# Kernel tuning notes

Hardware: AMD Instinct MI355X
Metric: run time of the kernel (lower is better)

The kernel has to match this reference:

```python
import jax, jax.numpy as jnp
import numpy as np

VOCAB, D, S, T, B, E, C = 21128, 768, 50, 5, 512, 128, 10


def gcn(x, edges, W, b):
    # GCNConv with self-loops and symmetric normalization. x: [S, D]
    N = x.shape[0]
    loop = jnp.arange(N)
    src = jnp.concatenate([edges[0], loop])
    dst = jnp.concatenate([edges[1], loop])
    deg = jax.ops.segment_sum(jnp.ones_like(src, dtype=x.dtype), dst, num_segments=N)
    dinv = jax.lax.rsqrt(jnp.maximum(deg, 1e-12))
    norm = dinv[src] * dinv[dst]
    h = x @ W  # [S, 10]
    out = jax.ops.segment_sum(h[src] * norm[:, None], dst, num_segments=N)
    return out + b


def mpm(self_f, cross_f, assign, W1, b1, W2, b2):
    # multi-perspective matching, broadcast over leading dims; node dim = -2
    a = assign * self_f
    c = assign * cross_f
    num = jnp.sum(a * c, axis=-1)
    den = jnp.maximum(jnp.linalg.norm(a, axis=-1) * jnp.linalg.norm(c, axis=-1), 1e-8)
    cos = num / den
    bshape = jnp.broadcast_shapes(self_f.shape[:-2], cross_f.shape[:-2])
    sf = jnp.broadcast_to(self_f, bshape + self_f.shape[-2:])
    h = jnp.concatenate([cos[..., None], sf], axis=-1)  # [..., S, 11]
    h = jax.nn.relu(h @ W1 + b1) @ W2 + b2  # [..., S, 20]
    return jnp.max(h, axis=-2)  # [..., 20]


def setup_inputs() -> dict:
    key = jax.random.key(0)
    ks = jax.random.split(key, 20)
    inp = {
        "context_input": jax.random.randint(ks[0], (B, T, S), 0, VOCAB),
        "response_input": jax.random.randint(ks[1], (B, S), 0, VOCAB),
        "context_graph_adjs": jax.random.randint(ks[2], (B, T, 2, E), 0, S),
        "response_graph_adj": jax.random.randint(ks[3], (B, 2, E), 0, S),
        "word_emb": jax.random.normal(ks[4], (VOCAB, D), jnp.float32) * 0.02,
        "conv_W": jax.random.normal(ks[5], (D, C), jnp.float32) * 0.05,
        "conv_b": jnp.zeros((C,), jnp.float32),
        "cross_w": jax.random.uniform(ks[6], (D, C), jnp.float32),
        "attention_coef": jax.random.uniform(ks[7], (S, S), jnp.float32),
        "assign_weight": jax.random.uniform(ks[8], (S, C), jnp.float32),
        "mp_W1": jax.random.normal(ks[9], (C + 1, 20), jnp.float32) * 0.3,
        "mp_b1": jnp.zeros((20,), jnp.float32),
        "mp_W2": jax.random.normal(ks[10], (20, 20), jnp.float32) * 0.2,
        "mp_b2": jnp.zeros((20,), jnp.float32),
        "ffn_W1": jax.random.normal(ks[11], (80, 40), jnp.float32) * 0.1,
        "ffn_b1": jnp.zeros((40,), jnp.float32),
        "ffn_W2": jax.random.normal(ks[12], (40, 1), jnp.float32) * 0.2,
        "ffn_b2": jnp.zeros((1,), jnp.float32),
    }
    return inp


def reference(context_input, response_input, context_graph_adjs, response_graph_adj,
              word_emb, conv_W, conv_b, cross_w, attention_coef, assign_weight,
              mp_W1, mp_b1, mp_W2, mp_b2, ffn_W1, ffn_b1, ffn_W2, ffn_b2):
    ctx = word_emb[context_input]      # [B, T, S, D]
    resp = word_emb[response_input]    # [B, S, D]

    gcn_b = jax.vmap(gcn, in_axes=(0, 0, None, None))
    resp_gcn = gcn_b(resp, response_graph_adj, conv_W, conv_b)                      # [B, S, C]
    ctx_gcn = jax.vmap(gcn_b, in_axes=(0, 0, None, None))(ctx, context_graph_adjs, conv_W, conv_b)  # [B, T, S, C]

    # cross features: utterance cross comes from response, response cross from utterance
    u_cross = jnp.einsum('ps,bsk->bpk', attention_coef, resp @ cross_w)   # [B, S, C]
    r_cross = jnp.einsum('ps,btsk->btpk', attention_coef, ctx @ cross_w)  # [B, T, S, C]

    g_u = mpm(ctx_gcn, u_cross[:, None], assign_weight, mp_W1, mp_b1, mp_W2, mp_b2)       # [B, T, 20]
    g_r = mpm(resp_gcn[:, None], r_cross, assign_weight, mp_W1, mp_b1, mp_W2, mp_b2)      # [B, T, 20]

    feat = jnp.concatenate([g_u, g_r, g_u * g_r, jnp.abs(g_u - g_r)], axis=-1)  # [B, T, 80]
    logits = jax.nn.relu(feat @ ffn_W1 + ffn_b1) @ ffn_W2 + ffn_b2              # [B, T, 1]
    return jax.nn.sigmoid(jnp.sum(logits, axis=1))                              # [B, 1]
```

## Files before the change

### kernel.cpp

```cpp
#include <hip/hip_runtime.h>
#include <math.h>

#define VOCAB 21128
#define DD 768
#define SS 50
#define TT 5
#define BB 512
#define EE 128
#define CC 10
#define V20 (VOCAB * 20)
#define NG 2560

__global__ __launch_bounds__(512) void k_vocab(const float* __restrict__ emb,
                                               const float* __restrict__ Wconv,
                                               const float* __restrict__ Wcross,
                                               float* __restrict__ hvp) {
    __shared__ float tile[8][64][21];
    const int wv = threadIdx.x >> 6, lane = threadIdx.x & 63;
    const int rowbase = blockIdx.x * 64;
    const int rsub = lane >> 2, m = lane & 3;

    float acc[20];
#pragma unroll
    for (int c = 0; c < 20; c++) acc[c] = 0.f;

    const int d0w = blockIdx.y * 384 + __builtin_amdgcn_readfirstlane(wv * 48);

    for (int chunk = 0; chunk < 3; ++chunk) {
        const int d0 = d0w + chunk * 16;
#pragma unroll
        for (int it = 0; it < 4; ++it) {
            int row = it * 16 + rsub;
            long r = rowbase + row;
            if (r >= VOCAB) r = VOCAB - 1;
            const float4 v = *(const float4*)(emb + r * DD + d0 + m * 4);
            tile[wv][row][m * 4 + 0] = v.x;
            tile[wv][row][m * 4 + 1] = v.y;
            tile[wv][row][m * 4 + 2] = v.z;
            tile[wv][row][m * 4 + 3] = v.w;
        }
#pragma unroll
        for (int d = 0; d < 16; ++d) {
            float e = tile[wv][lane][d];
            const float* wc = Wconv + (d0 + d) * 10;
            const float* wx = Wcross + (d0 + d) * 10;
#pragma unroll
            for (int c = 0; c < 10; c++) {
                acc[c] = fmaf(e, wc[c], acc[c]);
                acc[10 + c] = fmaf(e, wx[c], acc[10 + c]);
            }
        }
    }

    __syncthreads();
    float* pp = &tile[0][0][0];
#pragma unroll
    for (int c = 0; c < 20; c++) pp[wv * 1280 + lane * 20 + c] = acc[c];
    __syncthreads();
    float* outp = hvp + (long)blockIdx.y * V20;
    for (int i = threadIdx.x; i < 1280; i += 512) {
        int row = i / 20;
        long r = rowbase + row;
        if (r < VOCAB) {
            float s = 0.f;
#pragma unroll
            for (int w = 0; w < 8; ++w) s += pp[w * 1280 + i];
            outp[r * 20 + (i - row * 20)] = s;
        }
    }
}

__device__ __forceinline__ void wave_gcn(const int* __restrict__ tb,
                                         const int* __restrict__ ab,
                                         const float* __restrict__ hvp,
                                         const float* __restrict__ convb,
                                         const float (*attT)[51],
                                         float (*hsL)[21], float (*agg)[21], int* dgW,
                                         int lane, float* gcn, float* ax) {
    const int e1s = ab[lane], e2s = ab[lane + 64];
    const int e1d = ab[EE + lane], e2d = ab[EE + lane + 64];
    const int myTok = (lane < SS) ? tb[lane] : 0;

    dgW[lane] = 0;
    atomicAdd(&dgW[e1d], 1);
    atomicAdd(&dgW[e2d], 1);

    const float4* hv4 = (const float4*)hvp;
#pragma unroll
    for (int it = 0; it < 4; ++it) {
        const int idx = it * 64 + lane;
        int row = idx / 5;
        const int q = idx - row * 5;
        const int rowc = (row < SS) ? row : (SS - 1);
        const int t = __shfl(myTok, rowc);
        if (idx < SS * 5) {
            const float4 a = hv4[(long)t * 5 + q];
            const float4 bq = hv4[(long)(VOCAB * 5) + (long)t * 5 + q];
            float* dst = &hsL[row][q * 4];
            dst[0] = a.x + bq.x; dst[1] = a.y + bq.y;
            dst[2] = a.z + bq.z; dst[3] = a.w + bq.w;
        }
    }

    float dv = 0.f;
    if (lane < SS) dv = rsqrtf((float)(dgW[lane] + 1));

#pragma unroll
    for (int it = 0; it < 8; ++it) {
        const int i = it * 64 + lane;
        const int r = i / 10, c = i - r * 10;
        if (i < SS * 10) agg[r][c] = 0.f;
    }
    const float n1 = __shfl(dv, e1s) * __shfl(dv, e1d);
    const float n2 = __shfl(dv, e2s) * __shfl(dv, e2d);
#pragma unroll
    for (int c = 0; c < CC; c++) atomicAdd(&agg[e1d][c], hsL[e1s][c] * n1);
#pragma unroll
    for (int c = 0; c < CC; c++) atomicAdd(&agg[e2d][c], hsL[e2s][c] * n2);

    const int p = lane;
#pragma unroll
    for (int c = 0; c < CC; c++) { gcn[c] = 0.f; ax[c] = 0.f; }
    if (p < SS) {
        const float dp2 = dv * dv;
#pragma unroll
        for (int c = 0; c < CC; c++) gcn[c] = agg[p][c] + hsL[p][c] * dp2 + convb[c];
#pragma unroll 5
        for (int s = 0; s < SS; ++s) {
            const float a = attT[s][p];
#pragma unroll
            for (int c = 0; c < CC; c++) ax[c] = fmaf(a, hsL[s][10 + c], ax[c]);
        }
    }
}

__global__ __launch_bounds__(128) void k_resp(const int* __restrict__ rtok,
                                              const int* __restrict__ radj,
                                              const float* __restrict__ hvp,
                                              const float* __restrict__ convb,
                                              const float* __restrict__ att,
                                              float* __restrict__ srxu) {
    __shared__ float attT[SS][51];
    __shared__ float hsL[2][SS][21];
    __shared__ float aggL[2][SS][21];
    __shared__ int dgS[2][64];
    const int tid = threadIdx.x, wv = tid >> 6, lane = tid & 63;
    const int b = blockIdx.x * 2 + wv;

    for (int i = tid; i < SS * SS; i += 128) { int p = i / SS, s = i - p * SS; attT[s][p] = att[i]; }
    __syncthreads();

    float gcn[CC], ax[CC];
    wave_gcn(rtok + (long)b * SS, radj + (long)b * 2 * EE, hvp, convb, attT,
             hsL[wv], aggL[wv], dgS[wv], lane, gcn, ax);

    if (lane < SS) {
        float* o = srxu + (long)b * 1000 + lane * 20;
#pragma unroll
        for (int c = 0; c < CC; c++) { o[c] = gcn[c]; o[10 + c] = ax[c]; }
    }
}

__global__ __launch_bounds__(128) void k_utt(const int* __restrict__ ctok,
                                             const int* __restrict__ cadj,
                                             const float* __restrict__ hvp,
                                             const float* __restrict__ convb,
                                             const float* __restrict__ att,
                                             const float* __restrict__ assign,
                                             const float* __restrict__ W1, const float* __restrict__ b1,
                                             const float* __restrict__ W2, const float* __restrict__ b2,
                                             const float* __restrict__ srxu,
                                             float* __restrict__ guG,
                                             float* __restrict__ grG) {
    __shared__ float attT[SS][51];
    __shared__ float W2T[20][21];
    __shared__ float asgL[SS][11];
    __shared__ float hsL[2][SS][21];
    __shared__ float h1L[2][SS][21];
    __shared__ int dgS[2][64];
    const int tid = threadIdx.x, wv = tid >> 6, lane = tid & 63;
    const int g = blockIdx.x * 2 + wv;
    const int b = g / TT;

    for (int i = tid; i < SS * SS; i += 128) { int p = i / SS, s = i - p * SS; attT[s][p] = att[i]; }
    for (int i = tid; i < 400; i += 128) W2T[i % 20][i / 20] = W2[i];
    for (int i = tid; i < SS * CC; i += 128) asgL[i / CC][i % CC] = assign[i];
    __syncthreads();

    float gcn[CC], ax[CC];
    wave_gcn(ctok + (long)g * SS, cadj + (long)g * 2 * EE, hvp, convb, attT,
             hsL[wv], h1L[wv], dgS[wv], lane, gcn, ax);

    const int p = lane;
    float srv[CC], xuv[CC];
#pragma unroll
    for (int c = 0; c < CC; c++) { srv[c] = 0.f; xuv[c] = 0.f; }
    if (p < SS) {
        const float4* sp4 = (const float4*)(srxu + (long)b * 1000 + p * 20);
        const float4 t0 = sp4[0], t1 = sp4[1], t2 = sp4[2], t3 = sp4[3], t4 = sp4[4];
        srv[0] = t0.x; srv[1] = t0.y; srv[2] = t0.z; srv[3] = t0.w;
        srv[4] = t1.x; srv[5] = t1.y; srv[6] = t1.z; srv[7] = t1.w;
        srv[8] = t2.x; srv[9] = t2.y;
        xuv[0] = t2.z; xuv[1] = t2.w;
        xuv[2] = t3.x; xuv[3] = t3.y; xuv[4] = t3.z; xuv[5] = t3.w;
        xuv[6] = t4.x; xuv[7] = t4.y; xuv[8] = t4.z; xuv[9] = t4.w;
    }

    const int j = lane % 20;
    const int grp = lane / 20;
    float w2r[20];
#pragma unroll
    for (int k = 0; k < 20; k++) w2r[k] = W2T[j][k];

#pragma unroll
    for (int which = 0; which < 2; ++which) {
        if (p < SS) {
            float self[CC], cro[CC];
#pragma unroll
            for (int c = 0; c < CC; c++) {
                self[c] = which ? srv[c] : gcn[c];
                cro[c] = which ? ax[c] : xuv[c];
            }
            float num = 0.f, na = 0.f, nc2 = 0.f;
#pragma unroll
            for (int c = 0; c < CC; c++) {
                float av = asgL[p][c];
                float a = av * self[c];
                float cx = av * cro[c];
                num = fmaf(a, cx, num);
                na = fmaf(a, a, na);
                nc2 = fmaf(cx, cx, nc2);
            }
            float cosv = num / fmaxf(sqrtf(na) * sqrtf(nc2), 1e-8f);
            float h1[20];
#pragma unroll
            for (int q = 0; q < 20; q++) h1[q] = fmaf(cosv, W1[q], b1[q]);
#pragma unroll
            for (int k = 0; k < CC; k++) {
                float sv = self[k];
#pragma unroll
                for (int q = 0; q < 20; q++) h1[q] = fmaf(sv, W1[(k + 1) * 20 + q], h1[q]);
            }
#pragma unroll
            for (int q = 0; q < 20; q++) h1L[wv][p][q] = fmaxf(h1[q], 0.f);
        }

        float part = -1e30f;
        if (grp < 3) {
            const int s0 = grp * 17;
            const int s1 = (grp == 2) ? SS : (s0 + 17);
            for (int s = s0; s < s1; ++s) {
                float t = 0.f;
#pragma unroll
                for (int k = 0; k < 20; k++) t = fmaf(h1L[wv][s][k], w2r[k], t);
                part = fmaxf(part, t);
            }
        }
        const float a0 = __shfl(part, j);
        const float a1 = __shfl(part, j + 20);
        const float a2 = __shfl(part, j + 40);
        if (lane < 20) {
            float h2 = fmaxf(fmaxf(a0, a1), a2) + b2[lane];
            (which ? grG : guG)[(long)g * 20 + lane] = h2;
        }
    }
}

__global__ __launch_bounds__(64) void k_final(const float* __restrict__ g_u, const float* __restrict__ g_r,
                                              const float* __restrict__ W1, const float* __restrict__ b1,
                                              const float* __restrict__ W2, const float* __restrict__ b2,
                                              float* __restrict__ out) {
    const int b = blockIdx.x, lane = threadIdx.x;
    float ssum = 0.f;
    for (int t = 0; t < TT; t++) {
        const float* gu = g_u + ((long)b * TT + t) * 20;
        const float* gr = g_r + ((long)b * TT + t) * 20;
        float feat[80];
#pragma unroll
        for (int k = 0; k < 20; k++) {
            float u = gu[k], r = gr[k];
            feat[k] = u;
            feat[20 + k] = r;
            feat[40 + k] = u * r;
            feat[60 + k] = fabsf(u - r);
        }
        if (lane < 40) {
            float hv = b1[lane];
#pragma unroll
            for (int k = 0; k < 80; k++) hv = fmaf(feat[k], W1[k * 40 + lane], hv);
            ssum += fmaxf(hv, 0.f) * W2[lane];
        }
    }
    for (int off = 32; off; off >>= 1) ssum += __shfl_xor(ssum, off);
    if (lane == 0) out[b] = 1.f / (1.f + expf(-(ssum + (float)TT * b2[0])));
}

extern "C" void kernel_launch(void* const* d_in, const int* in_sizes, int n_in,
                              void* d_out, int out_size, void* d_ws, size_t ws_size,
                              hipStream_t stream) {
    (void)in_sizes; (void)n_in; (void)out_size; (void)ws_size;
    const int* ctx_tok = (const int*)d_in[0];
    const int* resp_tok = (const int*)d_in[1];
    const int* ctx_adj = (const int*)d_in[2];
    const int* resp_adj = (const int*)d_in[3];
    const float* emb = (const float*)d_in[4];
    const float* convW = (const float*)d_in[5];
    const float* convb = (const float*)d_in[6];
    const float* crossW = (const float*)d_in[7];
    const float* att = (const float*)d_in[8];
    const float* assign = (const float*)d_in[9];
    const float* mpW1 = (const float*)d_in[10];
    const float* mpb1 = (const float*)d_in[11];
    const float* mpW2 = (const float*)d_in[12];
    const float* mpb2 = (const float*)d_in[13];
    const float* fW1 = (const float*)d_in[14];
    const float* fb1 = (const float*)d_in[15];
    const float* fW2 = (const float*)d_in[16];
    const float* fb2 = (const float*)d_in[17];

    float* ws = (float*)d_ws;
    float* hvp = ws;
    float* srxu = hvp + 2 * V20;
    float* guG = srxu + (long)BB * 1000;
    float* grG = guG + (long)NG * 20;
    float* outf = (float*)d_out;

    hipLaunchKernelGGL(k_vocab, dim3((VOCAB + 63) / 64, 2), dim3(512), 0, stream,
                       emb, convW, crossW, hvp);
    hipLaunchKernelGGL(k_resp, dim3(BB / 2), dim3(128), 0, stream,
                       resp_tok, resp_adj, hvp, convb, att, srxu);
    hipLaunchKernelGGL(k_utt, dim3(NG / 2), dim3(128), 0, stream,
                       ctx_tok, ctx_adj, hvp, convb, att, assign,
                       mpW1, mpb1, mpW2, mpb2, srxu, guG, grG);
    hipLaunchKernelGGL(k_final, dim3(BB), dim3(64), 0, stream,
                       guG, grG, fW1, fb1, fW2, fb2, outf);
}
```

Baseline: 86.23 us.

## Split GCN and matching into separate kernels, prefetch vocab loads into registers

The response and utterance GCN work now runs in one kernel with four waves per block, writing per-node features to a workspace buffer. A separate matching kernel assigns one wave to each (group, perspective) pair instead of looping over both perspectives in one wave, which doubles wave-level parallelism. The vocab projection kernel issues all twelve float4 embedding loads up front before the compute loop, so more memory requests are in flight. The cost is an extra round trip through global memory for the GCN outputs, and more registers held in the vocab kernel.

```diff
diff --git a/kernel.cpp b/kernel.cpp
--- a/kernel.cpp
+++ b/kernel.cpp
@@ -10,6 +10,7 @@
 #define CC 10
 #define V20 (VOCAB * 20)
 #define NG 2560
+#define NALL 3072
 
 __global__ __launch_bounds__(512) void k_vocab(const float* __restrict__ emb,
                                                const float* __restrict__ Wconv,
@@ -20,24 +21,35 @@
     const int rowbase = blockIdx.x * 64;
     const int rsub = lane >> 2, m = lane & 3;
 
-    float acc[20];
-#pragma unroll
-    for (int c = 0; c < 20; c++) acc[c] = 0.f;
-
     const int d0w = blockIdx.y * 384 + __builtin_amdgcn_readfirstlane(wv * 48);
 
-    for (int chunk = 0; chunk < 3; ++chunk) {
-        const int d0 = d0w + chunk * 16;
+    float4 v[12];
+#pragma unroll
+    for (int ch = 0; ch < 3; ++ch) {
 #pragma unroll
         for (int it = 0; it < 4; ++it) {
             int row = it * 16 + rsub;
             long r = rowbase + row;
             if (r >= VOCAB) r = VOCAB - 1;
-            const float4 v = *(const float4*)(emb + r * DD + d0 + m * 4);
-            tile[wv][row][m * 4 + 0] = v.x;
-            tile[wv][row][m * 4 + 1] = v.y;
-            tile[wv][row][m * 4 + 2] = v.z;
-            tile[wv][row][m * 4 + 3] = v.w;
+            v[ch * 4 + it] = *(const float4*)(emb + r * DD + d0w + ch * 16 + m * 4);
+        }
+    }
+
+    float acc[20];
+#pragma unroll
+    for (int c = 0; c < 20; c++) acc[c] = 0.f;
+
+#pragma unroll
+    for (int ch = 0; ch < 3; ++ch) {
+        const int d0 = d0w + ch * 16;
+#pragma unroll
+        for (int it = 0; it < 4; ++it) {
+            const int row = it * 16 + rsub;
+            const float4 w = v[ch * 4 + it];
+            tile[wv][row][m * 4 + 0] = w.x;
+            tile[wv][row][m * 4 + 1] = w.y;
+            tile[wv][row][m * 4 + 2] = w.z;
+            tile[wv][row][m * 4 + 3] = w.w;
         }
 #pragma unroll
         for (int d = 0; d < 16; ++d) {
@@ -70,20 +82,37 @@
     }
 }
 
-__device__ __forceinline__ void wave_gcn(const int* __restrict__ tb,
-                                         const int* __restrict__ ab,
-                                         const float* __restrict__ hvp,
-                                         const float* __restrict__ convb,
-                                         const float (*attT)[51],
-                                         float (*hsL)[21], float (*agg)[21], int* dgW,
-                                         int lane, float* gcn, float* ax) {
+__global__ __launch_bounds__(256) void k_gcn(const int* __restrict__ ctok,
+                                             const int* __restrict__ cadj,
+                                             const int* __restrict__ rtok,
+                                             const int* __restrict__ radj,
+                                             const float* __restrict__ hvp,
+                                             const float* __restrict__ convb,
+                                             const float* __restrict__ att,
+                                             float* __restrict__ P) {
+    __shared__ float attT[SS][51];
+    __shared__ float hcv[4][SS][12];
+    __shared__ float hcx[4][SS][12];
+    __shared__ float aggL[4][SS][11];
+    __shared__ int dgS[4][64];
+    const int tid = threadIdx.x, wv = tid >> 6, lane = tid & 63;
+    const int G = blockIdx.x * 4 + wv;
+
+    for (int i = tid; i < SS * SS; i += 256) { int p = i / SS, s = i - p * SS; attT[s][p] = att[i]; }
+    __syncthreads();
+
+    const int* tb;
+    const int* ab;
+    if (G < NG) { tb = ctok + (long)G * SS; ab = cadj + (long)G * 2 * EE; }
+    else        { int b = G - NG; tb = rtok + (long)b * SS; ab = radj + (long)b * 2 * EE; }
+
     const int e1s = ab[lane], e2s = ab[lane + 64];
     const int e1d = ab[EE + lane], e2d = ab[EE + lane + 64];
     const int myTok = (lane < SS) ? tb[lane] : 0;
 
-    dgW[lane] = 0;
-    atomicAdd(&dgW[e1d], 1);
-    atomicAdd(&dgW[e2d], 1);
+    dgS[wv][lane] = 0;
+    atomicAdd(&dgS[wv][e1d], 1);
+    atomicAdd(&dgS[wv][e2d], 1);
 
     const float4* hv4 = (const float4*)hvp;
 #pragma unroll
@@ -95,115 +124,107 @@
         const int t = __shfl(myTok, rowc);
         if (idx < SS * 5) {
             const float4 a = hv4[(long)t * 5 + q];
-            const float4 bq = hv4[(long)(VOCAB * 5) + (long)t * 5 + q];
-            float* dst = &hsL[row][q * 4];
-            dst[0] = a.x + bq.x; dst[1] = a.y + bq.y;
-            dst[2] = a.z + bq.z; dst[3] = a.w + bq.w;
+            const float4 b = hv4[(long)(VOCAB * 5) + (long)t * 5 + q];
+            const float4 w = make_float4(a.x + b.x, a.y + b.y, a.z + b.z, a.w + b.w);
+            if (q == 0)      *(float4*)&hcv[wv][row][0] = w;
+            else if (q == 1) *(float4*)&hcv[wv][row][4] = w;
+            else if (q == 2) { hcv[wv][row][8] = w.x; hcv[wv][row][9] = w.y;
+                               hcx[wv][row][0] = w.z; hcx[wv][row][1] = w.w; }
+            else if (q == 3) { *(float2*)&hcx[wv][row][2] = make_float2(w.x, w.y);
+                               *(float2*)&hcx[wv][row][4] = make_float2(w.z, w.w); }
+            else             { *(float2*)&hcx[wv][row][6] = make_float2(w.x, w.y);
+                               *(float2*)&hcx[wv][row][8] = make_float2(w.z, w.w); }
         }
     }
 
     float dv = 0.f;
-    if (lane < SS) dv = rsqrtf((float)(dgW[lane] + 1));
-
-#pragma unroll
-    for (int it = 0; it < 8; ++it) {
-        const int i = it * 64 + lane;
-        const int r = i / 10, c = i - r * 10;
-        if (i < SS * 10) agg[r][c] = 0.f;
-    }
+    if (lane < SS) dv = rsqrtf((float)(dgS[wv][lane] + 1));
+
+    float* aggW = &aggL[wv][0][0];
+    for (int i = lane; i < SS * 11; i += 64) aggW[i] = 0.f;
     const float n1 = __shfl(dv, e1s) * __shfl(dv, e1d);
     const float n2 = __shfl(dv, e2s) * __shfl(dv, e2d);
 #pragma unroll
-    for (int c = 0; c < CC; c++) atomicAdd(&agg[e1d][c], hsL[e1s][c] * n1);
-#pragma unroll
-    for (int c = 0; c < CC; c++) atomicAdd(&agg[e2d][c], hsL[e2s][c] * n2);
+    for (int c = 0; c < CC; c++) atomicAdd(&aggW[e1d * 11 + c], hcv[wv][e1s][c] * n1);
+#pragma unroll
+    for (int c = 0; c < CC; c++) atomicAdd(&aggW[e2d * 11 + c], hcv[wv][e2s][c] * n2);
 
     const int p = lane;
-#pragma unroll
-    for (int c = 0; c < CC; c++) { gcn[c] = 0.f; ax[c] = 0.f; }
     if (p < SS) {
+        float gcn[CC], ax[CC];
         const float dp2 = dv * dv;
-#pragma unroll
-        for (int c = 0; c < CC; c++) gcn[c] = agg[p][c] + hsL[p][c] * dp2 + convb[c];
+        const float4 s0 = *(const float4*)&hcv[wv][p][0];
+        const float4 s1 = *(const float4*)&hcv[wv][p][4];
+        const float s8 = hcv[wv][p][8], s9 = hcv[wv][p][9];
+        gcn[0] = aggW[p * 11 + 0] + s0.x * dp2 + convb[0];
+        gcn[1] = aggW[p * 11 + 1] + s0.y * dp2 + convb[1];
+        gcn[2] = aggW[p * 11 + 2] + s0.z * dp2 + convb[2];
+        gcn[3] = aggW[p * 11 + 3] + s0.w * dp2 + convb[3];
+        gcn[4] = aggW[p * 11 + 4] + s1.x * dp2 + convb[4];
+        gcn[5] = aggW[p * 11 + 5] + s1.y * dp2 + convb[5];
+        gcn[6] = aggW[p * 11 + 6] + s1.z * dp2 + convb[6];
+        gcn[7] = aggW[p * 11 + 7] + s1.w * dp2 + convb[7];
+        gcn[8] = aggW[p * 11 + 8] + s8 * dp2 + convb[8];
+        gcn[9] = aggW[p * 11 + 9] + s9 * dp2 + convb[9];
+#pragma unroll
+        for (int c = 0; c < CC; c++) ax[c] = 0.f;
 #pragma unroll 5
         for (int s = 0; s < SS; ++s) {
             const float a = attT[s][p];
-#pragma unroll
-            for (int c = 0; c < CC; c++) ax[c] = fmaf(a, hsL[s][10 + c], ax[c]);
-        }
-    }
-}
-
-__global__ __launch_bounds__(128) void k_resp(const int* __restrict__ rtok,
-                                              const int* __restrict__ radj,
-                                              const float* __restrict__ hvp,
-                                              const float* __restrict__ convb,
-                                              const float* __restrict__ att,
-                                              float* __restrict__ srxu) {
-    __shared__ float attT[SS][51];
-    __shared__ float hsL[2][SS][21];
-    __shared__ float aggL[2][SS][21];
-    __shared__ int dgS[2][64];
-    const int tid = threadIdx.x, wv = tid >> 6, lane = tid & 63;
-    const int b = blockIdx.x * 2 + wv;
-
-    for (int i = tid; i < SS * SS; i += 128) { int p = i / SS, s = i - p * SS; attT[s][p] = att[i]; }
-    __syncthreads();
-
-    float gcn[CC], ax[CC];
-    wave_gcn(rtok + (long)b * SS, radj + (long)b * 2 * EE, hvp, convb, attT,
-             hsL[wv], aggL[wv], dgS[wv], lane, gcn, ax);
-
-    if (lane < SS) {
-        float* o = srxu + (long)b * 1000 + lane * 20;
-#pragma unroll
-        for (int c = 0; c < CC; c++) { o[c] = gcn[c]; o[10 + c] = ax[c]; }
-    }
-}
-
-__global__ __launch_bounds__(128) void k_utt(const int* __restrict__ ctok,
-                                             const int* __restrict__ cadj,
-                                             const float* __restrict__ hvp,
-                                             const float* __restrict__ convb,
-                                             const float* __restrict__ att,
+            const float4 x0 = *(const float4*)&hcx[wv][s][0];
+            const float4 x1 = *(const float4*)&hcx[wv][s][4];
+            const float2 x2 = *(const float2*)&hcx[wv][s][8];
+            ax[0] = fmaf(a, x0.x, ax[0]); ax[1] = fmaf(a, x0.y, ax[1]);
+            ax[2] = fmaf(a, x0.z, ax[2]); ax[3] = fmaf(a, x0.w, ax[3]);
+            ax[4] = fmaf(a, x1.x, ax[4]); ax[5] = fmaf(a, x1.y, ax[5]);
+            ax[6] = fmaf(a, x1.z, ax[6]); ax[7] = fmaf(a, x1.w, ax[7]);
+            ax[8] = fmaf(a, x2.x, ax[8]); ax[9] = fmaf(a, x2.y, ax[9]);
+        }
+        float4* o4 = (float4*)(P + (long)G * 1000 + p * 20);
+        o4[0] = make_float4(gcn[0], gcn[1], gcn[2], gcn[3]);
+        o4[1] = make_float4(gcn[4], gcn[5], gcn[6], gcn[7]);
+        o4[2] = make_float4(gcn[8], gcn[9], ax[0], ax[1]);
+        o4[3] = make_float4(ax[2], ax[3], ax[4], ax[5]);
+        o4[4] = make_float4(ax[6], ax[7], ax[8], ax[9]);
+    }
+}
+
+__global__ __launch_bounds__(256) void k_mpm(const float* __restrict__ P,
                                              const float* __restrict__ assign,
                                              const float* __restrict__ W1, const float* __restrict__ b1,
                                              const float* __restrict__ W2, const float* __restrict__ b2,
-                                             const float* __restrict__ srxu,
                                              float* __restrict__ guG,
                                              float* __restrict__ grG) {
-    __shared__ float attT[SS][51];
     __shared__ float W2T[20][21];
     __shared__ float asgL[SS][11];
-    __shared__ float hsL[2][SS][21];
-    __shared__ float h1L[2][SS][21];
-    __shared__ int dgS[2][64];
+    __shared__ float h1L[4][SS][20];
     const int tid = threadIdx.x, wv = tid >> 6, lane = tid & 63;
-    const int g = blockIdx.x * 2 + wv;
+    const int wid = blockIdx.x * 4 + wv;
+    const int g = wid >> 1, which = wid & 1;
     const int b = g / TT;
 
-    for (int i = tid; i < SS * SS; i += 128) { int p = i / SS, s = i - p * SS; attT[s][p] = att[i]; }
-    for (int i = tid; i < 400; i += 128) W2T[i % 20][i / 20] = W2[i];
-    for (int i = tid; i < SS * CC; i += 128) asgL[i / CC][i % CC] = assign[i];
+    for (int i = tid; i < 400; i += 256) W2T[i % 20][i / 20] = W2[i];
+    for (int i = tid; i < SS * CC; i += 256) asgL[i / CC][i % CC] = assign[i];
     __syncthreads();
 
-    float gcn[CC], ax[CC];
-    wave_gcn(ctok + (long)g * SS, cadj + (long)g * 2 * EE, hvp, convb, attT,
-             hsL[wv], h1L[wv], dgS[wv], lane, gcn, ax);
+    const float* Pc = P + (long)g * 1000;
+    const float* Pr = P + (long)(NG + b) * 1000;
+    const float* selfP = which ? Pr : Pc;
+    const float* croP  = which ? Pc : Pr;
 
     const int p = lane;
-    float srv[CC], xuv[CC];
-#pragma unroll
-    for (int c = 0; c < CC; c++) { srv[c] = 0.f; xuv[c] = 0.f; }
+    float self[CC], cro[CC];
     if (p < SS) {
-        const float4* sp4 = (const float4*)(srxu + (long)b * 1000 + p * 20);
-        const float4 t0 = sp4[0], t1 = sp4[1], t2 = sp4[2], t3 = sp4[3], t4 = sp4[4];
-        srv[0] = t0.x; srv[1] = t0.y; srv[2] = t0.z; srv[3] = t0.w;
-        srv[4] = t1.x; srv[5] = t1.y; srv[6] = t1.z; srv[7] = t1.w;
-        srv[8] = t2.x; srv[9] = t2.y;
-        xuv[0] = t2.z; xuv[1] = t2.w;
-        xuv[2] = t3.x; xuv[3] = t3.y; xuv[4] = t3.z; xuv[5] = t3.w;
-        xuv[6] = t4.x; xuv[7] = t4.y; xuv[8] = t4.z; xuv[9] = t4.w;
+        const float4* s4 = (const float4*)(selfP + p * 20);
+        const float4 a0 = s4[0], a1 = s4[1], a2 = s4[2];
+        self[0] = a0.x; self[1] = a0.y; self[2] = a0.z; self[3] = a0.w;
+        self[4] = a1.x; self[5] = a1.y; self[6] = a1.z; self[7] = a1.w;
+        self[8] = a2.x; self[9] = a2.y;
+        const float4* c4 = (const float4*)(croP + p * 20);
+        const float4 b0 = c4[2], b1q = c4[3], b2q = c4[4];
+        cro[0] = b0.z; cro[1] = b0.w;
+        cro[2] = b1q.x; cro[3] = b1q.y; cro[4] = b1q.z; cro[5] = b1q.w;
+        cro[6] = b2q.x; cro[7] = b2q.y; cro[8] = b2q.z; cro[9] = b2q.w;
     }
 
     const int j = lane % 20;
@@ -212,57 +233,53 @@
 #pragma unroll
     for (int k = 0; k < 20; k++) w2r[k] = W2T[j][k];
 
-#pragma unroll
-    for (int which = 0; which < 2; ++which) {
-        if (p < SS) {
-            float self[CC], cro[CC];
-#pragma unroll
-            for (int c = 0; c < CC; c++) {
-                self[c] = which ? srv[c] : gcn[c];
-                cro[c] = which ? ax[c] : xuv[c];
-            }
-            float num = 0.f, na = 0.f, nc2 = 0.f;
-#pragma unroll
-            for (int c = 0; c < CC; c++) {
-                float av = asgL[p][c];
-                float a = av * self[c];
-                float cx = av * cro[c];
-                num = fmaf(a, cx, num);
-                na = fmaf(a, a, na);
-                nc2 = fmaf(cx, cx, nc2);
-            }
-            float cosv = num / fmaxf(sqrtf(na) * sqrtf(nc2), 1e-8f);
-            float h1[20];
-#pragma unroll
-            for (int q = 0; q < 20; q++) h1[q] = fmaf(cosv, W1[q], b1[q]);
-#pragma unroll
-            for (int k = 0; k < CC; k++) {
-                float sv = self[k];
-#pragma unroll
-                for (int q = 0; q < 20; q++) h1[q] = fmaf(sv, W1[(k + 1) * 20 + q], h1[q]);
-            }
-#pragma unroll
-            for (int q = 0; q < 20; q++) h1L[wv][p][q] = fmaxf(h1[q], 0.f);
-        }
-
-        float part = -1e30f;
-        if (grp < 3) {
-            const int s0 = grp * 17;
-            const int s1 = (grp == 2) ? SS : (s0 + 17);
-            for (int s = s0; s < s1; ++s) {
-                float t = 0.f;
-#pragma unroll
-                for (int k = 0; k < 20; k++) t = fmaf(h1L[wv][s][k], w2r[k], t);
-                part = fmaxf(part, t);
-            }
-        }
-        const float a0 = __shfl(part, j);
-        const float a1 = __shfl(part, j + 20);
-        const float a2 = __shfl(part, j + 40);
-        if (lane < 20) {
-            float h2 = fmaxf(fmaxf(a0, a1), a2) + b2[lane];
-            (which ? grG : guG)[(long)g * 20 + lane] = h2;
-        }
+    if (p < SS) {
+        float num = 0.f, na = 0.f, nc2 = 0.f;
+#pragma unroll
+        for (int c = 0; c < CC; c++) {
+            float av = asgL[p][c];
+            float a = av * self[c];
+            float cx = av * cro[c];
+            num = fmaf(a, cx, num);
+            na = fmaf(a, a, na);
+            nc2 = fmaf(cx, cx, nc2);
+        }
+        float cosv = num / fmaxf(sqrtf(na) * sqrtf(nc2), 1e-8f);
+        float h1[20];
+#pragma unroll
+        for (int q = 0; q < 20; q++) h1[q] = fmaf(cosv, W1[q], b1[q]);
+#pragma unroll
+        for (int k = 0; k < CC; k++) {
+            float sv = self[k];
+#pragma unroll
+            for (int q = 0; q < 20; q++) h1[q] = fmaf(sv, W1[(k + 1) * 20 + q], h1[q]);
+        }
+        float4* hw = (float4*)&h1L[wv][p][0];
+        hw[0] = make_float4(fmaxf(h1[0], 0.f), fmaxf(h1[1], 0.f), fmaxf(h1[2], 0.f), fmaxf(h1[3], 0.f));
+        hw[1] = make_float4(fmaxf(h1[4], 0.f), fmaxf(h1[5], 0.f), fmaxf(h1[6], 0.f), fmaxf(h1[7], 0.f));
+        hw[2] = make_float4(fmaxf(h1[8], 0.f), fmaxf(h1[9], 0.f), fmaxf(h1[10], 0.f), fmaxf(h1[11], 0.f));
+        hw[3] = make_float4(fmaxf(h1[12], 0.f), fmaxf(h1[13], 0.f), fmaxf(h1[14], 0.f), fmaxf(h1[15], 0.f));
+        hw[4] = make_float4(fmaxf(h1[16], 0.f), fmaxf(h1[17], 0.f), fmaxf(h1[18], 0.f), fmaxf(h1[19], 0.f));
+    }
+
+    float part = -1e30f;
+    if (grp < 3) {
+        const int s0 = grp * 17;
+        const int s1 = (grp == 2) ? SS : (s0 + 17);
+        for (int s = s0; s < s1; ++s) {
+            const float* hr = &h1L[wv][s][0];
+            float t = 0.f;
+#pragma unroll
+            for (int k = 0; k < 20; k++) t = fmaf(hr[k], w2r[k], t);
+            part = fmaxf(part, t);
+        }
+    }
+    const float a0 = __shfl(part, j);
+    const float a1 = __shfl(part, j + 20);
+    const float a2 = __shfl(part, j + 40);
+    if (lane < 20) {
+        float h2 = fmaxf(fmaxf(a0, a1), a2) + b2[lane];
+        (which ? grG : guG)[(long)g * 20 + lane] = h2;
     }
 }
 
@@ -320,18 +337,17 @@
 
     float* ws = (float*)d_ws;
     float* hvp = ws;
-    float* srxu = hvp + 2 * V20;
-    float* guG = srxu + (long)BB * 1000;
+    float* P = hvp + 2 * V20;
+    float* guG = P + (long)NALL * 1000;
     float* grG = guG + (long)NG * 20;
     float* outf = (float*)d_out;
 
     hipLaunchKernelGGL(k_vocab, dim3((VOCAB + 63) / 64, 2), dim3(512), 0, stream,
                        emb, convW, crossW, hvp);
-    hipLaunchKernelGGL(k_resp, dim3(BB / 2), dim3(128), 0, stream,
-                       resp_tok, resp_adj, hvp, convb, att, srxu);
-    hipLaunchKernelGGL(k_utt, dim3(NG / 2), dim3(128), 0, stream,
-                       ctx_tok, ctx_adj, hvp, convb, att, assign,
-                       mpW1, mpb1, mpW2, mpb2, srxu, guG, grG);
+    hipLaunchKernelGGL(k_gcn, dim3(NALL / 4), dim3(256), 0, stream,
+                       ctx_tok, ctx_adj, resp_tok, resp_adj, hvp, convb, att, P);
+    hipLaunchKernelGGL(k_mpm, dim3(NG * 2 / 4), dim3(256), 0, stream,
+                       P, assign, mpW1, mpb1, mpW2, mpb2, guG, grG);
     hipLaunchKernelGGL(k_final, dim3(BB), dim3(64), 0, stream,
                        guG, grG, fW1, fb1, fW2, fb2, outf);
 }
```

Result: faster. 79.22 us (-8.1%).
